# Optimization experiments

Hardware: AMD Instinct MI355X
Metric: run time of the kernel (lower is better)

## Reference

```python
import jax, jax.numpy as jnp
import numpy as np

B, S, D = 2, 2048, 1024
H, DK = 16, 64  # num_heads, key_dim (value_dim defaults to key_dim)


def setup_inputs() -> dict:
    key = jax.random.key(0)
    ks = jax.random.split(key, 11)
    init = lambda k, shape, fan_in: jax.random.uniform(
        k, shape, jnp.float32, -1.0, 1.0) * (1.0 / np.sqrt(fan_in))
    return {
        "query": jax.random.normal(ks[0], (B, S, D), jnp.float32),
        "key": jax.random.normal(ks[1], (B, S, D), jnp.float32),
        "value": jax.random.normal(ks[2], (B, S, D), jnp.float32),
        "Wq": init(ks[3], (D, H, DK), D),
        "bq": jnp.zeros((H, DK), jnp.float32),
        "Wk": init(ks[4], (D, H, DK), D),
        "bk": jnp.zeros((H, DK), jnp.float32),
        "Wv": init(ks[5], (D, H, DK), D),
        "bv": jnp.zeros((H, DK), jnp.float32),
        "Wo": init(ks[6], (H, DK, D), H * DK),
        "bo": jnp.zeros((D,), jnp.float32),
    }


def reference(query, key, value, Wq, bq, Wk, bk, Wv, bv, Wo, bo):
    # QKV projections: abc,cde->abde (EinsumDense with bias on (H, DK))
    q = jnp.einsum("bsd,dhk->bshk", query, Wq) + bq  # [B,S,H,DK]
    k = jnp.einsum("bsd,dhk->bshk", key, Wk) + bk
    v = jnp.einsum("bsd,dhk->bshk", value, Wv) + bv
    # Keras scales the query before the dot product
    q = q * (1.0 / jnp.sqrt(jnp.asarray(DK, q.dtype)))
    # aecd,abcd->acbe : [B,H,Sq,Sk]
    scores = jnp.einsum("bqhk,bshk->bhqs", q, k)
    probs = jax.nn.softmax(scores, axis=-1)
    # acbe,aecd->abcd : [B,Sq,H,DK]
    attn = jnp.einsum("bhqs,bshk->bqhk", probs, v)
    # output projection: abcd,cde->abe
    out = jnp.einsum("bqhk,hkd->bqd", attn, Wo) + bo  # [B,S,D]
    return out
```

## Files before the change

kernel.cpp:

```cpp
#include <hip/hip_runtime.h>
#include <hip/hip_bf16.h>
#include <stdint.h>
#include <stddef.h>


typedef __bf16 bf16;
typedef __attribute__((ext_vector_type(4))) bf16 bf16x4;
typedef __attribute__((ext_vector_type(8))) bf16 bf16x8;
typedef __attribute__((ext_vector_type(4))) float f32x4;
typedef __attribute__((ext_vector_type(16))) float f32x16;
typedef __attribute__((ext_vector_type(2))) unsigned int uint2v;

#define DEVINL static __device__ __forceinline__

DEVINL void gload_lds16(const void* g, void* l) {
  __builtin_amdgcn_global_load_lds(
      (const __attribute__((address_space(1))) void*)g,
      (__attribute__((address_space(3))) void*)l, 16, 0, 0);
}

DEVINL f32x4 mfma16(bf16x8 a, bf16x8 b, f32x4 c) {
  return __builtin_amdgcn_mfma_f32_16x16x32_bf16(a, b, c, 0, 0, 0);
}
DEVINL f32x16 mfma32(bf16x8 a, bf16x8 b, f32x16 c) {
  return __builtin_amdgcn_mfma_f32_32x32x16_bf16(a, b, c, 0, 0, 0);
}
DEVINL float fexp2(float x) {
  float r;
  asm("v_exp_f32 %0, %1" : "=v"(r) : "v"(x));
  return r;
}
DEVINL unsigned pack2(float lo, float hi) {
  union { bf16 h[2]; unsigned u; } t;
  t.h[0] = (bf16)lo; t.h[1] = (bf16)hi;
  return t.u;
}
DEVINL bf16x8 mk8(unsigned a, unsigned b, unsigned c, unsigned d) {
  union { unsigned u[4]; bf16x8 v; } t;
  t.u[0] = a; t.u[1] = b; t.u[2] = c; t.u[3] = d;
  return t.v;
}

__global__ __launch_bounds__(256) void wt_kernel(
    const float* __restrict__ w0, const float* __restrict__ w1,
    const float* __restrict__ w2, const float* __restrict__ w3,
    bf16* __restrict__ out) {
  __shared__ float tile[64 * 65];
  int t = blockIdx.y;
  const float* w = (t == 0) ? w0 : (t == 1) ? w1 : (t == 2) ? w2 : w3;
  bf16* o = out + (size_t)t * 1024 * 1024;
  int tb = blockIdx.x;
  int k0 = (tb >> 4) * 64, n0 = (tb & 15) * 64;
  int c = threadIdx.x & 63, r0 = threadIdx.x >> 6;
  for (int r = r0; r < 64; r += 4)
    tile[r * 65 + c] = w[(size_t)(k0 + r) * 1024 + n0 + c];
  __syncthreads();
  for (int r = r0; r < 64; r += 4)
    o[(size_t)(n0 + r) * 1024 + k0 + c] = (bf16)tile[c * 65 + r];
}

__global__ __launch_bounds__(256) void gemm_qkv(
    const float* __restrict__ Aq, const float* __restrict__ Ak,
    const float* __restrict__ Av, const bf16* __restrict__ Wt,
    const float* __restrict__ bq, const float* __restrict__ bk,
    const float* __restrict__ bv,
    bf16* __restrict__ outQ, bf16* __restrict__ outK, bf16* __restrict__ Vt) {
  int z = blockIdx.z;
  const float* A   = (z == 0) ? Aq : (z == 1) ? Ak : Av;
  const bf16* Wz   = Wt + (size_t)z * 1024 * 1024;
  const float* bia = (z == 0) ? bq : (z == 1) ? bk : bv;
  float scale      = (z == 0) ? 0.18033688011112042f : 1.0f;

  __shared__ float Af[2][4096];
  __shared__ bf16  Bs[2][128 * 32];

  int m0 = blockIdx.x * 128, n0 = blockIdx.y * 128;
  int tid = threadIdx.x, w = tid >> 6, l = tid & 63;
  int wm = (w >> 1) * 64, wn = (w & 1) * 64;
  int c16 = l & 15, g = l >> 4;
  int rsw = (c16 >> 1) & 3;

  int ua[4], ar[4], aso[4];
#pragma unroll
  for (int i = 0; i < 4; ++i) {
    ua[i] = (w * 4 + i) * 64 + l;
    int rr = (ua[i] >> 2) & 127;
    int cc = (ua[i] & 3) ^ ((rr >> 1) & 3);
    ar[i] = rr;
    aso[i] = ((ua[i] >> 9) << 4) + cc * 4;
  }
  int brow0 = (w * 2 + 0) * 16 + (l >> 2);
  int brow1 = (w * 2 + 1) * 16 + (l >> 2);
  int bk0 = ((l & 3) ^ ((brow0 >> 1) & 3)) * 8;
  int bk1 = ((l & 3) ^ ((brow1 >> 1) & 3)) * 8;

  f32x4 acc[4][4] = {};

#define STAGE_QKV(buf, kt)                                                   \
  do {                                                                       \
    _Pragma("unroll") for (int i = 0; i < 4; ++i)                            \
      gload_lds16(A + (size_t)(m0 + ar[i]) * 1024 + (kt) + aso[i],           \
                  (char*)Af[buf] + ua[i] * 16);                              \
    gload_lds16(Wz + (size_t)(n0 + brow0) * 1024 + (kt) + bk0,               \
                (char*)Bs[buf] + (w * 2 + 0) * 1024 + l * 16);               \
    gload_lds16(Wz + (size_t)(n0 + brow1) * 1024 + (kt) + bk1,               \
                (char*)Bs[buf] + (w * 2 + 1) * 1024 + l * 16);               \
  } while (0)

  STAGE_QKV(0, 0);
  __syncthreads();

  int cur = 0;
  for (int kt = 0; kt < 1024; kt += 32) {
    if (kt < 992) STAGE_QKV(cur ^ 1, kt + 32);
    bf16x8 af[4], bfr[4];
#pragma unroll
    for (int mt = 0; mt < 4; ++mt) {
      int row = wm + mt * 16 + c16;
      int base = ((g >> 1) << 11) + row * 16;
      f32x4 lo = *(const f32x4*)&Af[cur][base + ((((g & 1) * 2)     ^ rsw) << 2)];
      f32x4 hi = *(const f32x4*)&Af[cur][base + ((((g & 1) * 2 + 1) ^ rsw) << 2)];
      bf16x8 h;
#pragma unroll
      for (int j = 0; j < 4; ++j) { h[j] = (bf16)lo[j]; h[4 + j] = (bf16)hi[j]; }
      af[mt] = h;
    }
#pragma unroll
    for (int nt = 0; nt < 4; ++nt)
      bfr[nt] = *(const bf16x8*)&Bs[cur][(wn + nt * 16 + c16) * 32 + ((g ^ rsw) * 8)];
#pragma unroll
    for (int mt = 0; mt < 4; ++mt)
#pragma unroll
      for (int nt = 0; nt < 4; ++nt)
        acc[mt][nt] = mfma16(af[mt], bfr[nt], acc[mt][nt]);
    __syncthreads();
    cur ^= 1;
  }
#undef STAGE_QKV

  if (z < 2) {
    bf16* Cout = (z == 0) ? outQ : outK;
#pragma unroll
    for (int mt = 0; mt < 4; ++mt)
#pragma unroll
      for (int nt = 0; nt < 4; ++nt) {
        int n = n0 + wn + nt * 16 + c16;
        float bb = bia[n];
#pragma unroll
        for (int r = 0; r < 4; ++r) {
          int m = m0 + wm + mt * 16 + g * 4 + r;
          Cout[(size_t)m * 1024 + n] = (bf16)((acc[mt][nt][r] + bb) * scale);
        }
      }
  } else {
#pragma unroll
    for (int mt = 0; mt < 4; ++mt)
#pragma unroll
      for (int nt = 0; nt < 4; ++nt) {
        int n = n0 + wn + nt * 16 + c16;
        float bb = bia[n];
        int m = m0 + wm + mt * 16 + g * 4;
        int b = m >> 11, s = m & 2047;
        bf16x4 v;
#pragma unroll
        for (int r = 0; r < 4; ++r) v[r] = (bf16)(acc[mt][nt][r] + bb);
        *(bf16x4*)&Vt[((size_t)(b * 16 + (n >> 6)) * 64 + (n & 63)) * 2048 + s] = v;
      }
  }
}

__global__ __launch_bounds__(256, 2) void flash_kernel(
    const bf16* __restrict__ Qp, const bf16* __restrict__ Kp,
    const bf16* __restrict__ Vt, bf16* __restrict__ AO) {
  __shared__ __align__(16) bf16 Ks[4][64 * 64];
  __shared__ __align__(16) bf16 Vs[4][64 * 64];

  int orig = blockIdx.x;
  int wg = (orig & 7) * 64 + (orig >> 3);
  int bh = wg >> 4, qb = wg & 15;
  int b = bh >> 4, h = bh & 15;
  int tid = threadIdx.x, w = tid >> 6, l = tid & 63;
  int lo5 = l & 31, g = l >> 5;
  int q0 = qb * 128 + w * 32;

  const bf16* qptr = Qp + (size_t)(b * 2048 + q0 + lo5) * 1024 + h * 64 + g * 8;
  bf16x8 qf0 = *(const bf16x8*)(qptr + 0);
  bf16x8 qf1 = *(const bf16x8*)(qptr + 16);
  bf16x8 qf2 = *(const bf16x8*)(qptr + 32);
  bf16x8 qf3 = *(const bf16x8*)(qptr + 48);

  const bf16* kbase = Kp + (size_t)(b * 2048) * 1024 + h * 64;
  const bf16* vbase = Vt + (size_t)bh * 64 * 2048;

  int un = w * 64 + l;
  int ur = un >> 2;
  int uc = (un & 3) ^ ((ur >> 1) & 3);
  int ub = un * 8;
  int swr = (lo5 >> 1) & 3;

#define STAGE(buf, s0)                                                          \
  do {                                                                          \
    gload_lds16(kbase + (size_t)((s0) + ur) * 1024 + uc * 8,                    \
                (bf16*)Ks[buf] + ub);                                           \
    gload_lds16(kbase + (size_t)((s0) + ur) * 1024 + 32 + uc * 8,               \
                (bf16*)Ks[buf] + 2048 + ub);                                    \
    gload_lds16(vbase + (size_t)ur * 2048 + (s0) + uc * 8,                      \
                (bf16*)Vs[buf] + ub);                                           \
    gload_lds16(vbase + (size_t)ur * 2048 + (s0) + 32 + uc * 8,                 \
                (bf16*)Vs[buf] + 2048 + ub);                                    \
  } while (0)

#define LDSK(cp, nt, kt)                                                        \
  (*(const bf16x8*)&cp[(((kt) >> 1) << 11) + (((nt)*32 + lo5) << 5) +           \
                       (((((kt)*2 + g) & 3) ^ swr) << 3)])
#define LDSV(cp, dt, st)                                                        \
  (*(const bf16x8*)&cp[(((st) >> 1) << 11) + (((dt)*32 + lo5) << 5) +           \
                       (((((st)*2 + g) & 3) ^ swr) << 3)])

#define QK(d0, d1, kc)                                                          \
  do {                                                                          \
    __builtin_amdgcn_s_setprio(1);                                              \
    d0 = z16; d1 = z16;                                                         \
    d0 = mfma32(LDSK(kc, 0, 0), qf0, d0);                                       \
    d0 = mfma32(LDSK(kc, 0, 1), qf1, d0);                                       \
    d0 = mfma32(LDSK(kc, 0, 2), qf2, d0);                                       \
    d0 = mfma32(LDSK(kc, 0, 3), qf3, d0);                                       \
    d1 = mfma32(LDSK(kc, 1, 0), qf0, d1);                                       \
    d1 = mfma32(LDSK(kc, 1, 1), qf1, d1);                                       \
    d1 = mfma32(LDSK(kc, 1, 2), qf2, d1);                                       \
    d1 = mfma32(LDSK(kc, 1, 3), qf3, d1);                                       \
    __builtin_amdgcn_s_setprio(0);                                              \
  } while (0)

#define SOFTMAX(sv, sw)                                                         \
  do {                                                                          \
    float p[16];                                                                \
    _Pragma("unroll") for (int r = 0; r < 16; ++r) p[r] = fexp2(sv[r]);         \
    ps0 += p[0] + p[4] + p[8] + p[12];                                          \
    ps1 += p[1] + p[5] + p[9] + p[13];                                          \
    ps2 += p[2] + p[6] + p[10] + p[14];                                         \
    ps3 += p[3] + p[7] + p[11] + p[15];                                         \
    unsigned pw0 = pack2(p[0], p[1]), pw1 = pack2(p[2], p[3]);                  \
    unsigned pw2 = pack2(p[4], p[5]), pw3 = pack2(p[6], p[7]);                  \
    unsigned pw4 = pack2(p[8], p[9]), pw5 = pack2(p[10], p[11]);                \
    unsigned pw6 = pack2(p[12], p[13]), pw7 = pack2(p[14], p[15]);              \
    uint2v a02 = __builtin_amdgcn_permlane32_swap(pw0, pw2, false, false);      \
    uint2v a13 = __builtin_amdgcn_permlane32_swap(pw1, pw3, false, false);      \
    uint2v a46 = __builtin_amdgcn_permlane32_swap(pw4, pw6, false, false);      \
    uint2v a57 = __builtin_amdgcn_permlane32_swap(pw5, pw7, false, false);      \
    pa0 = mk8(a02.x, a13.x, a02.y, a13.y);                                      \
    pa1 = mk8(a46.x, a57.x, a46.y, a57.y);                                      \
    _Pragma("unroll") for (int r = 0; r < 16; ++r) p[r] = fexp2(sw[r]);         \
    ps0 += p[0] + p[4] + p[8] + p[12];                                          \
    ps1 += p[1] + p[5] + p[9] + p[13];                                          \
    ps2 += p[2] + p[6] + p[10] + p[14];                                         \
    ps3 += p[3] + p[7] + p[11] + p[15];                                         \
    pw0 = pack2(p[0], p[1]); pw1 = pack2(p[2], p[3]);                           \
    pw2 = pack2(p[4], p[5]); pw3 = pack2(p[6], p[7]);                           \
    pw4 = pack2(p[8], p[9]); pw5 = pack2(p[10], p[11]);                         \
    pw6 = pack2(p[12], p[13]); pw7 = pack2(p[14], p[15]);                       \
    a02 = __builtin_amdgcn_permlane32_swap(pw0, pw2, false, false);             \
    a13 = __builtin_amdgcn_permlane32_swap(pw1, pw3, false, false);             \
    a46 = __builtin_amdgcn_permlane32_swap(pw4, pw6, false, false);             \
    a57 = __builtin_amdgcn_permlane32_swap(pw5, pw7, false, false);             \
    pb0 = mk8(a02.x, a13.x, a02.y, a13.y);                                      \
    pb1 = mk8(a46.x, a57.x, a46.y, a57.y);                                      \
  } while (0)

#define PV(vc)                                                                  \
  do {                                                                          \
    __builtin_amdgcn_s_setprio(1);                                              \
    o0 = mfma32(pa0, LDSV(vc, 0, 0), o0);                                       \
    o1 = mfma32(pa0, LDSV(vc, 1, 0), o1);                                       \
    o0 = mfma32(pa1, LDSV(vc, 0, 1), o0);                                       \
    o1 = mfma32(pa1, LDSV(vc, 1, 1), o1);                                       \
    o0 = mfma32(pb0, LDSV(vc, 0, 2), o0);                                       \
    o1 = mfma32(pb0, LDSV(vc, 1, 2), o1);                                       \
    o0 = mfma32(pb1, LDSV(vc, 0, 3), o0);                                       \
    o1 = mfma32(pb1, LDSV(vc, 1, 3), o1);                                       \
    __builtin_amdgcn_s_setprio(0);                                              \
  } while (0)

  const f32x16 z16 = {};
  f32x16 o0 = z16, o1 = z16;
  f32x16 sA0, sA1, sB0, sB1;
  bf16x8 pa0, pa1, pb0, pb1;
  float ps0 = 0.f, ps1 = 0.f, ps2 = 0.f, ps3 = 0.f;

  STAGE(0, 0);
  STAGE(1, 64);
  asm volatile("s_waitcnt vmcnt(6)" ::: "memory");
  __builtin_amdgcn_s_barrier();
  __builtin_amdgcn_sched_barrier(0);
  QK(sA0, sA1, Ks[0]);

  for (int t = 0; t < 32; t += 2) {
    if (t < 30) {
      STAGE((t + 2) & 3, (t + 2) * 64);
      asm volatile("s_waitcnt vmcnt(6)" ::: "memory");
    } else {
      asm volatile("s_waitcnt vmcnt(2)" ::: "memory");
    }
    __builtin_amdgcn_s_barrier();
    __builtin_amdgcn_sched_barrier(0);
    QK(sB0, sB1, Ks[(t + 1) & 3]);
    SOFTMAX(sA0, sA1);
    PV(Vs[t & 3]);

    if (t < 29) {
      STAGE((t + 3) & 3, (t + 3) * 64);
      asm volatile("s_waitcnt vmcnt(6)" ::: "memory");
    } else {
      asm volatile("s_waitcnt vmcnt(0)" ::: "memory");
    }
    __builtin_amdgcn_s_barrier();
    __builtin_amdgcn_sched_barrier(0);
    if (t < 30) QK(sA0, sA1, Ks[(t + 2) & 3]);
    SOFTMAX(sB0, sB1);
    PV(Vs[(t + 1) & 3]);
  }
#undef STAGE
#undef LDSK
#undef LDSV
#undef QK
#undef SOFTMAX
#undef PV

  float plsum = (ps0 + ps1) + (ps2 + ps3);
  float tot = plsum + __shfl_xor(plsum, 32);

#pragma unroll
  for (int r = 0; r < 16; ++r) {
    int qr = (r & 3) + 8 * (r >> 2) + 4 * g;
    float inv = 1.0f / __shfl(tot, qr);
    bf16* op = AO + (size_t)(b * 2048 + q0 + qr) * 1024 + h * 64 + lo5;
    op[0]  = (bf16)(o0[r] * inv);
    op[32] = (bf16)(o1[r] * inv);
  }
}

__global__ __launch_bounds__(256) void gemm_o(
    const bf16* __restrict__ A, const bf16* __restrict__ Wt3,
    const float* __restrict__ bo, float* __restrict__ C) {
  __shared__ bf16 As[2][64 * 32];
  __shared__ bf16 Bs[2][128 * 32];
  int m0 = blockIdx.x * 64, n0 = blockIdx.y * 128;
  int tid = threadIdx.x, w = tid >> 6, l = tid & 63;
  int wm = (w >> 1) * 32, wn = (w & 1) * 64;
  int c16 = l & 15, g = l >> 4;
  int rsw = (c16 >> 1) & 3;

  int arow = tid >> 2, akc = tid & 3;
  int asrc = (akc ^ ((arow >> 1) & 3)) * 8;
  int brow0 = (w * 2 + 0) * 16 + (l >> 2);
  int brow1 = (w * 2 + 1) * 16 + (l >> 2);
  int bk0 = ((l & 3) ^ ((brow0 >> 1) & 3)) * 8;
  int bk1 = ((l & 3) ^ ((brow1 >> 1) & 3)) * 8;

  f32x4 acc[2][4] = {};

#define STAGE_O(buf, kt)                                                     \
  do {                                                                       \
    gload_lds16(A + (size_t)(m0 + arow) * 1024 + (kt) + asrc,                \
                (char*)As[buf] + tid * 16);                                  \
    gload_lds16(Wt3 + (size_t)(n0 + brow0) * 1024 + (kt) + bk0,              \
                (char*)Bs[buf] + (w * 2 + 0) * 1024 + l * 16);               \
    gload_lds16(Wt3 + (size_t)(n0 + brow1) * 1024 + (kt) + bk1,              \
                (char*)Bs[buf] + (w * 2 + 1) * 1024 + l * 16);               \
  } while (0)

  STAGE_O(0, 0);
  __syncthreads();

  int cur = 0;
  for (int kt = 0; kt < 1024; kt += 32) {
    if (kt < 992) STAGE_O(cur ^ 1, kt + 32);
    bf16x8 af[2], bfr[4];
#pragma unroll
    for (int mt = 0; mt < 2; ++mt)
      af[mt] = *(const bf16x8*)&As[cur][(wm + mt * 16 + c16) * 32 + ((g ^ rsw) * 8)];
#pragma unroll
    for (int nt = 0; nt < 4; ++nt)
      bfr[nt] = *(const bf16x8*)&Bs[cur][(wn + nt * 16 + c16) * 32 + ((g ^ rsw) * 8)];
#pragma unroll
    for (int mt = 0; mt < 2; ++mt)
#pragma unroll
      for (int nt = 0; nt < 4; ++nt)
        acc[mt][nt] = mfma16(af[mt], bfr[nt], acc[mt][nt]);
    __syncthreads();
    cur ^= 1;
  }
#undef STAGE_O

#pragma unroll
  for (int mt = 0; mt < 2; ++mt)
#pragma unroll
    for (int nt = 0; nt < 4; ++nt) {
      int n = n0 + wn + nt * 16 + c16;
      float bb = bo[n];
#pragma unroll
      for (int r = 0; r < 4; ++r) {
        int m = m0 + wm + mt * 16 + g * 4 + r;
        C[(size_t)m * 1024 + n] = acc[mt][nt][r] + bb;
      }
    }
}

extern "C" void kernel_launch(void* const* d_in, const int* in_sizes, int n_in,
                              void* d_out, int out_size, void* d_ws, size_t ws_size,
                              hipStream_t stream) {
  const float* query = (const float*)d_in[0];
  const float* key_  = (const float*)d_in[1];
  const float* value = (const float*)d_in[2];
  const float* Wq = (const float*)d_in[3];
  const float* bq = (const float*)d_in[4];
  const float* Wk = (const float*)d_in[5];
  const float* bk = (const float*)d_in[6];
  const float* Wv = (const float*)d_in[7];
  const float* bv = (const float*)d_in[8];
  const float* Wo = (const float*)d_in[9];
  const float* bo = (const float*)d_in[10];
  float* out = (float*)d_out;

  char* ws = (char*)d_ws;
  const size_t MB = 1024 * 1024;
  bf16* Wt  = (bf16*)(ws);
  bf16* Qp  = (bf16*)(ws + 8 * MB);
  bf16* Kp  = (bf16*)(ws + 16 * MB);
  bf16* Vt  = (bf16*)(ws + 24 * MB);
  bf16* AO  = (bf16*)(ws + 32 * MB);

  wt_kernel<<<dim3(256, 4), dim3(256), 0, stream>>>(Wq, Wk, Wv, Wo, Wt);
  gemm_qkv<<<dim3(32, 8, 3), dim3(256), 0, stream>>>(query, key_, value, Wt,
                                                     bq, bk, bv, Qp, Kp, Vt);
  flash_kernel<<<dim3(512), dim3(256), 0, stream>>>(Qp, Kp, Vt, AO);
  gemm_o<<<dim3(64, 8), dim3(256), 0, stream>>>(AO, Wt + (size_t)3 * 1024 * 1024, bo, out);
}
```

Baseline: 124.8 us.

## Triple-buffer QKV projection GEMM with explicit vmcnt waits and XOR swizzle tweak

Moves the QKV projection GEMM from double to triple buffering in LDS, so loads run two k-tiles ahead of compute. __syncthreads is replaced by explicit s_waitcnt vmcnt counts, raw s_barrier and sched_barrier, which keeps later loads in flight while the current tile is consumed. The A-tile swizzle also XORs in the half index, which is meant to reduce LDS bank conflicts. LDS use rises by half, which may lower occupancy. The hand-counted vmcnt values must match the number of loads issued per stage.

After: 141.3 us. +13.2%, slower.

```diff
diff --git a/kernel.cpp b/kernel.cpp
--- a/kernel.cpp
+++ b/kernel.cpp
@@ -71,23 +71,25 @@
   const float* bia = (z == 0) ? bq : (z == 1) ? bk : bv;
   float scale      = (z == 0) ? 0.18033688011112042f : 1.0f;
 
-  __shared__ float Af[2][4096];
-  __shared__ bf16  Bs[2][128 * 32];
+  __shared__ float Af[3][4096];
+  __shared__ bf16  Bs[3][128 * 32];
 
   int m0 = blockIdx.x * 128, n0 = blockIdx.y * 128;
   int tid = threadIdx.x, w = tid >> 6, l = tid & 63;
   int wm = (w >> 1) * 64, wn = (w & 1) * 64;
   int c16 = l & 15, g = l >> 4;
   int rsw = (c16 >> 1) & 3;
+  int ghf = g >> 1;
 
   int ua[4], ar[4], aso[4];
 #pragma unroll
   for (int i = 0; i < 4; ++i) {
     ua[i] = (w * 4 + i) * 64 + l;
+    int hf = ua[i] >> 9;
     int rr = (ua[i] >> 2) & 127;
-    int cc = (ua[i] & 3) ^ ((rr >> 1) & 3);
+    int cc = (ua[i] & 3) ^ ((rr >> 1) & 3) ^ hf;
     ar[i] = rr;
-    aso[i] = ((ua[i] >> 9) << 4) + cc * 4;
+    aso[i] = hf * 16 + cc * 4;
   }
   int brow0 = (w * 2 + 0) * 16 + (l >> 2);
   int brow1 = (w * 2 + 1) * 16 + (l >> 2);
@@ -108,18 +110,30 @@
   } while (0)
 
   STAGE_QKV(0, 0);
-  __syncthreads();
-
-  int cur = 0;
-  for (int kt = 0; kt < 1024; kt += 32) {
-    if (kt < 992) STAGE_QKV(cur ^ 1, kt + 32);
+  STAGE_QKV(1, 32);
+
+  for (int t = 0; t < 32; ++t) {
+    if (t < 30) {
+      STAGE_QKV((t + 2) % 3, (t + 2) * 32);
+      asm volatile("s_waitcnt vmcnt(12)" ::: "memory");
+    } else if (t == 30) {
+      asm volatile("s_waitcnt vmcnt(6)" ::: "memory");
+    } else {
+      asm volatile("s_waitcnt vmcnt(0)" ::: "memory");
+    }
+    __builtin_amdgcn_s_barrier();
+    __builtin_amdgcn_sched_barrier(0);
+
+    const int cur = t % 3;
     bf16x8 af[4], bfr[4];
 #pragma unroll
     for (int mt = 0; mt < 4; ++mt) {
       int row = wm + mt * 16 + c16;
-      int base = ((g >> 1) << 11) + row * 16;
-      f32x4 lo = *(const f32x4*)&Af[cur][base + ((((g & 1) * 2)     ^ rsw) << 2)];
-      f32x4 hi = *(const f32x4*)&Af[cur][base + ((((g & 1) * 2 + 1) ^ rsw) << 2)];
+      int base = (ghf << 11) + row * 16;
+      int pl = (((g & 1) * 2)     ^ rsw ^ ghf) << 2;
+      int ph = (((g & 1) * 2 + 1) ^ rsw ^ ghf) << 2;
+      f32x4 lo = *(const f32x4*)&Af[cur][base + pl];
+      f32x4 hi = *(const f32x4*)&Af[cur][base + ph];
       bf16x8 h;
 #pragma unroll
       for (int j = 0; j < 4; ++j) { h[j] = (bf16)lo[j]; h[4 + j] = (bf16)hi[j]; }
@@ -133,8 +147,9 @@
 #pragma unroll
       for (int nt = 0; nt < 4; ++nt)
         acc[mt][nt] = mfma16(af[mt], bfr[nt], acc[mt][nt]);
-    __syncthreads();
-    cur ^= 1;
+
+    __builtin_amdgcn_sched_barrier(0);
+    __builtin_amdgcn_s_barrier();
   }
 #undef STAGE_QKV
 
```
